# Kernel optimization log

Measured on AMD Instinct MI355X. Metric: run time of the kernel, lower is better.

The kernel has to match this reference:

```python
import jax, jax.numpy as jnp
import numpy as np

B, T, P, J, DIN, H, DOUT = 8, 64, 8, 32, 6, 256, 9
N = P * J


def _glorot(key, shape):
    fan_in, fan_out = shape[0], shape[1]
    s = jnp.sqrt(2.0 / (fan_in + fan_out)).astype(jnp.float32)
    return jax.random.normal(key, shape, jnp.float32) * s


def setup_inputs() -> dict:
    key = jax.random.key(0)
    ks = jax.random.split(key, 12)
    x2d = jax.random.normal(ks[0], (B, T, P, J, DIN), jnp.float32)
    mask = jnp.ones((B, T, P, J, 1), jnp.float32)
    # sparse-ish symmetric spatial adjacency with self loops, row-normalized
    a = (jax.random.uniform(ks[1], (N, N)) < 0.05).astype(jnp.float32)
    a = jnp.maximum(a, a.T) + jnp.eye(N, dtype=jnp.float32)
    s_adj = a / jnp.sum(a, axis=1, keepdims=True)
    return {
        "x2d": x2d,
        "mask": mask,
        "s_adj": s_adj,
        # layer 0: dim_in -> H, gates packed [z | r | c]
        "Wx0": _glorot(ks[2], (DIN, 3 * H)),
        "Wh0": _glorot(ks[3], (H, 3 * H)),
        "b0": jnp.zeros((3 * H,), jnp.float32),
        # layer 1: H -> H
        "Wx1": _glorot(ks[4], (H, 3 * H)),
        "Wh1": _glorot(ks[5], (H, 3 * H)),
        "b1": jnp.zeros((3 * H,), jnp.float32),
        # output head
        "Wout": _glorot(ks[6], (H, DOUT)),
        "bout": jnp.zeros((DOUT,), jnp.float32),
    }


def _gcgru_layer(xs, s_adj, Wx, Wh, b):
    """xs: [B, T, N, D] -> hidden sequence [B, T, N, H]."""
    h_dim = Wh.shape[0]

    def step(h, x_t):
        # graph conv of input and hidden state: A @ (.)
        Ax = jnp.einsum('nm,bmd->bnd', s_adj, x_t)          # [B,N,D]
        Ah = jnp.einsum('nm,bmh->bnh', s_adj, h)            # [B,N,H]
        gx = Ax @ Wx + b                                    # [B,N,3H]
        gzr = gx[..., : 2 * h_dim] + Ah @ Wh[:, : 2 * h_dim]
        z = jax.nn.sigmoid(gzr[..., :h_dim])                # update gate
        r = jax.nn.sigmoid(gzr[..., h_dim:])                # reset gate
        Arh = jnp.einsum('nm,bmh->bnh', s_adj, r * h)       # conv of reset hidden
        c = jnp.tanh(gx[..., 2 * h_dim:] + Arh @ Wh[:, 2 * h_dim:])
        h_new = z * h + (1.0 - z) * c
        return h_new, h_new

    h0 = jnp.zeros((xs.shape[0], xs.shape[2], h_dim), xs.dtype)
    _, hs = jax.lax.scan(step, h0, jnp.moveaxis(xs, 1, 0))  # hs: [T,B,N,H]
    return jnp.moveaxis(hs, 0, 1)


def reference(x2d, mask, s_adj, Wx0, Wh0, b0, Wx1, Wh1, b1, Wout, bout):
    bsz, seq_len, num_p, num_j, din = x2d.shape
    xs = (x2d * mask).reshape(bsz, seq_len, num_p * num_j, din)
    xs = _gcgru_layer(xs, s_adj, Wx0, Wh0, b0)
    xs = _gcgru_layer(xs, s_adj, Wx1, Wh1, b1)
    ys = xs @ Wout + bout                                   # [B,T,N,DOUT]
    return ys.reshape(bsz, seq_len, num_p, num_j, -1)
```

## Files before the change

### kernel.cpp

```cpp
#include <hip/hip_runtime.h>
#include <math.h>


#define BB 8
#define TT 64
#define NN 256
#define HH 256
#define BN 2048
#define LSTR 72

typedef float f32x4 __attribute__((ext_vector_type(4)));
typedef short s16x8 __attribute__((ext_vector_type(8)));

#define MFMA(a, b, c) __builtin_amdgcn_mfma_f32_16x16x32_bf16(a, b, c, 0, 0, 0)

__device__ __forceinline__ ushort rne_bf16(float x) {
    unsigned u = __builtin_bit_cast(unsigned, x);
    unsigned r = u + 0x7FFFu + ((u >> 16) & 1u);
    return (ushort)(r >> 16);
}
__device__ __forceinline__ float bf16_f32(ushort h) {
    unsigned u = ((unsigned)h) << 16;
    return __builtin_bit_cast(float, u);
}
__device__ __forceinline__ void split2(float x, ushort& hi, ushort& lo) {
    ushort h = rne_bf16(x);
    hi = h;
    lo = rne_bf16(x - bf16_f32(h));
}

__global__ __launch_bounds__(256) void prep_kernel(const float* __restrict__ A,
    const float* __restrict__ Wh0, const float* __restrict__ Wx1,
    const float* __restrict__ Wh1,
    ushort* Abf, ushort* WzrT0, ushort* WcT0, ushort* WxzrT1,
    ushort* WhzrT1, ushort* WxcT1, ushort* WhcT1)
{
    int idx = blockIdx.x * 256 + threadIdx.x;
    if (idx < 65536) { Abf[idx] = rne_bf16(A[idx]); return; }
    int e = idx - 65536;
    ushort* dst; const float* src; int colOff;
    if      (e < 131072) { dst = WzrT0;  src = Wh0; colOff = 0;   }
    else if (e < 196608) { dst = WcT0;   src = Wh0; colOff = 512; e -= 131072; }
    else if (e < 327680) { dst = WxzrT1; src = Wx1; colOff = 0;   e -= 196608; }
    else if (e < 458752) { dst = WhzrT1; src = Wh1; colOff = 0;   e -= 327680; }
    else if (e < 524288) { dst = WxcT1;  src = Wx1; colOff = 512; e -= 458752; }
    else if (e < 589824) { dst = WhcT1;  src = Wh1; colOff = 512; e -= 524288; }
    else return;
    int c = e >> 8, k = e & 255;
    dst[e] = rne_bf16(src[k * 768 + colOff + c]);
}

__device__ void x_job(int lb, int tid, float* xs, float* red, const float* Af,
                      const float* x2d, const float* mask, float* Ax0, int t) {
    int b = lb >> 2, rt = lb & 3;
    const float* xbase = x2d + ((size_t)(b * TT + t) * NN) * 6;
    const float* mbase = mask + (size_t)(b * TT + t) * NN;
    {
        int m = tid;
        float mk = mbase[m];
        #pragma unroll
        for (int d = 0; d < 6; ++d) xs[m * 8 + d] = xbase[m * 6 + d] * mk;
    }
    __syncthreads();
    int i = tid & 63, q = tid >> 6;
    const float* arow = Af + (size_t)(rt * 64 + i) * 256 + q * 64;
    float a6[6] = {0.f, 0.f, 0.f, 0.f, 0.f, 0.f};
    for (int m = 0; m < 64; ++m) {
        float a = arow[m];
        const float* xv = &xs[(q * 64 + m) * 8];
        #pragma unroll
        for (int d = 0; d < 6; ++d) a6[d] = fmaf(a, xv[d], a6[d]);
    }
    #pragma unroll
    for (int d = 0; d < 6; ++d) red[(i * 4 + q) * 8 + d] = a6[d];
    __syncthreads();
    for (int idx2 = tid; idx2 < 64 * 6; idx2 += 256) {
        int ii = idx2 / 6, d = idx2 - ii * 6;
        float s = red[(ii * 4 + 0) * 8 + d] + red[(ii * 4 + 1) * 8 + d]
                + red[(ii * 4 + 2) * 8 + d] + red[(ii * 4 + 3) * 8 + d];
        Ax0[(size_t)(b * 256 + rt * 64 + ii) * 8 + d] = s;
    }
}

__device__ void head_job(int lb, int tid, const float* h1, const float* Wout,
                         const float* bout, float* out, int tprev) {
    int g = lb * 256 + tid;
    int row = g / 9, o = g - row * 9;
    if (row >= BN) return;
    const float* hr = h1 + (size_t)row * 256;
    float s = bout[o];
    for (int k = 0; k < 256; k += 4) {
        float4 hv = *(const float4*)(hr + k);
        s = fmaf(hv.x, Wout[(k + 0) * 9 + o], s);
        s = fmaf(hv.y, Wout[(k + 1) * 9 + o], s);
        s = fmaf(hv.z, Wout[(k + 2) * 9 + o], s);
        s = fmaf(hv.w, Wout[(k + 3) * 9 + o], s);
    }
    int b = row >> 8, n = row & 255;
    out[((size_t)(b * TT + tprev) * NN + n) * 9 + o] = s;
}

__global__ __launch_bounds__(256) void head_kernel(const float* __restrict__ h1,
    const float* __restrict__ Wout, const float* __restrict__ bout,
    float* __restrict__ out, int tprev)
{
    head_job(blockIdx.x, threadIdx.x, h1, Wout, bout, out, tprev);
}

struct G2P {
    const ushort* Abf;
    const ushort* XThi0; const ushort* XTlo0; ushort* Yhi0; ushort* Ylo0;
    const ushort* XThi1; const ushort* XTlo1; ushort* Yhi1; ushort* Ylo1;
    int nJobs;
    int doX;
    int headT;
    int t;
    const float* Af; const float* x2d; const float* mask; float* Ax0;
    const float* h1; const float* Wout; const float* bout; float* out;
};

__global__ __launch_bounds__(256) void g2_kernel(G2P p) {
    __shared__ ushort lds[3 * 64 * LSTR];
    ushort* As   = lds;
    ushort* Bshi = lds + 64 * LSTR;
    ushort* Bslo = lds + 2 * 64 * LSTR;
    const int tid = threadIdx.x;
    const int bid = blockIdx.x;
    const int mainB = p.nJobs * 128;

    if (bid < mainB) {
        const int job = bid >> 7, lb = bid & 127;
        const ushort* XThi = job ? p.XThi1 : p.XThi0;
        const ushort* XTlo = job ? p.XTlo1 : p.XTlo0;
        ushort* Yhi = job ? p.Yhi1 : p.Yhi0;
        ushort* Ylo = job ? p.Ylo1 : p.Ylo0;
        const int b = lb >> 4, rt = (lb >> 2) & 3, ct = lb & 3;

        const int lane = tid & 63, wave = tid >> 6;
        const int wr = wave >> 1, wc = wave & 1;
        const int l15 = lane & 15, q8 = (lane >> 4) << 3;

        f32x4 acc[2][2];
        acc[0][0] = 0.f; acc[0][1] = 0.f; acc[1][0] = 0.f; acc[1][1] = 0.f;

        const int rr = tid >> 2, ko = (tid & 3) << 4;
        const ushort* Asrc = p.Abf + (size_t)(rt * 64 + rr) * 256 + ko;
        const ushort* Bh   = XThi + (size_t)(b * 256 + ct * 64 + rr) * 256 + ko;
        const ushort* Bl   = XTlo + (size_t)(b * 256 + ct * 64 + rr) * 256 + ko;
        ushort* wA = &As[rr * LSTR + ko];
        ushort* wH = &Bshi[rr * LSTR + ko];
        ushort* wL = &Bslo[rr * LSTR + ko];

        uint4 rA0 = *(const uint4*)(Asrc);
        uint4 rA1 = *(const uint4*)(Asrc + 8);
        uint4 rH0 = *(const uint4*)(Bh);
        uint4 rH1 = *(const uint4*)(Bh + 8);
        uint4 rL0 = *(const uint4*)(Bl);
        uint4 rL1 = *(const uint4*)(Bl + 8);

        for (int k0 = 0; k0 < 256; k0 += 64) {
            __syncthreads();
            *(uint4*)(wA)     = rA0;
            *(uint4*)(wA + 8) = rA1;
            *(uint4*)(wH)     = rH0;
            *(uint4*)(wH + 8) = rH1;
            *(uint4*)(wL)     = rL0;
            *(uint4*)(wL + 8) = rL1;
            __syncthreads();
            if (k0 < 192) {
                rA0 = *(const uint4*)(Asrc + k0 + 64);
                rA1 = *(const uint4*)(Asrc + k0 + 72);
                rH0 = *(const uint4*)(Bh + k0 + 64);
                rH1 = *(const uint4*)(Bh + k0 + 72);
                rL0 = *(const uint4*)(Bl + k0 + 64);
                rL1 = *(const uint4*)(Bl + k0 + 72);
            }
            #pragma unroll
            for (int sub = 0; sub < 2; ++sub) {
                const int kb = sub * 32 + q8;
                s16x8 a0  = *(const s16x8*)&As[(wr * 32 + l15) * LSTR + kb];
                s16x8 a1  = *(const s16x8*)&As[(wr * 32 + 16 + l15) * LSTR + kb];
                s16x8 bh0 = *(const s16x8*)&Bshi[(wc * 32 + l15) * LSTR + kb];
                s16x8 bh1 = *(const s16x8*)&Bshi[(wc * 32 + 16 + l15) * LSTR + kb];
                s16x8 bl0 = *(const s16x8*)&Bslo[(wc * 32 + l15) * LSTR + kb];
                s16x8 bl1 = *(const s16x8*)&Bslo[(wc * 32 + 16 + l15) * LSTR + kb];
                acc[0][0] = MFMA(a0, bh0, acc[0][0]);
                acc[0][0] = MFMA(a0, bl0, acc[0][0]);
                acc[0][1] = MFMA(a0, bh1, acc[0][1]);
                acc[0][1] = MFMA(a0, bl1, acc[0][1]);
                acc[1][0] = MFMA(a1, bh0, acc[1][0]);
                acc[1][0] = MFMA(a1, bl0, acc[1][0]);
                acc[1][1] = MFMA(a1, bh1, acc[1][1]);
                acc[1][1] = MFMA(a1, bl1, acc[1][1]);
            }
        }
        const int quad = lane >> 4;
        #pragma unroll
        for (int i = 0; i < 2; ++i) {
            #pragma unroll
            for (int j = 0; j < 2; ++j) {
                const int col = ct * 64 + wc * 32 + j * 16 + l15;
                const int m0  = rt * 64 + wr * 32 + i * 16 + quad * 4;
                const size_t base = (size_t)(b * 256 + m0) * 256 + col;
                #pragma unroll
                for (int r = 0; r < 4; ++r) {
                    ushort hi, lo;
                    split2(acc[i][j][r], hi, lo);
                    Yhi[base + (size_t)r * 256] = hi;
                    Ylo[base + (size_t)r * 256] = lo;
                }
            }
        }
    } else if (bid < mainB + 32) {
        if (p.doX)
            x_job(bid - mainB, tid, (float*)lds, (float*)(lds + 64 * LSTR),
                  p.Af, p.x2d, p.mask, p.Ax0, p.t);
    } else {
        if (p.headT >= 0)
            head_job(bid - mainB - 32, tid, p.h1, p.Wout, p.bout, p.out, p.headT);
    }
}

struct WSub {
    const ushort* Lhi0; const ushort* Llo0; const ushort* RT0;
    const ushort* Lhi1; const ushort* Llo1; const ushort* RT1;
    int ngemm;
    const float* bias;
    int useK6; int wxColOff;
    const float* h;
    float* z;
    float* hOut;
    ushort* Thi; ushort* Tlo;
};

struct WAP2 {
    WSub u0, u1;
    int nBlk0;
    int mode;
    const float* Ax0; const float* Wx0;
};

__global__ __launch_bounds__(256) void wact_kernel(WAP2 p) {
    __shared__ ushort lds[3 * 64 * LSTR];
    ushort* Ashi = lds;
    ushort* Aslo = lds + 64 * LSTR;
    ushort* Bs   = lds + 2 * 64 * LSTR;
    const int tid = threadIdx.x;
    const int bid = blockIdx.x;
    const int isU1 = (bid >= p.nBlk0);
    const WSub u = isU1 ? p.u1 : p.u0;
    const int lb = isU1 ? bid - p.nBlk0 : bid;
    int b, rt, ct;
    if (p.mode == 0) { b = lb >> 5; rt = (lb >> 3) & 3; ct = lb & 7; }
    else             { b = lb >> 4; rt = (lb >> 2) & 3; ct = lb & 3; }

    const int lane = tid & 63, wave = tid >> 6;
    const int wr = wave >> 1, wc = wave & 1;
    const int l15 = lane & 15, q8 = (lane >> 4) << 3;

    f32x4 acc[2][2];
    acc[0][0] = 0.f; acc[0][1] = 0.f; acc[1][0] = 0.f; acc[1][1] = 0.f;

    const int rr = tid >> 2, ko = (tid & 3) << 4;
    for (int g = 0; g < u.ngemm; ++g) {
        const ushort* Lh = (g ? u.Lhi1 : u.Lhi0) + (size_t)(b * 256 + rt * 64 + rr) * 256 + ko;
        const ushort* Ll = (g ? u.Llo1 : u.Llo0) + (size_t)(b * 256 + rt * 64 + rr) * 256 + ko;
        const ushort* Rt = (g ? u.RT1  : u.RT0 ) + (size_t)(ct * 64 + rr) * 256 + ko;
        ushort* wA = &Ashi[rr * LSTR + ko];
        ushort* wL = &Aslo[rr * LSTR + ko];
        ushort* wB = &Bs[rr * LSTR + ko];

        uint4 rA0 = *(const uint4*)(Lh);
        uint4 rA1 = *(const uint4*)(Lh + 8);
        uint4 rL0 = *(const uint4*)(Ll);
        uint4 rL1 = *(const uint4*)(Ll + 8);
        uint4 rB0 = *(const uint4*)(Rt);
        uint4 rB1 = *(const uint4*)(Rt + 8);

        for (int k0 = 0; k0 < 256; k0 += 64) {
            __syncthreads();
            *(uint4*)(wA)     = rA0;
            *(uint4*)(wA + 8) = rA1;
            *(uint4*)(wL)     = rL0;
            *(uint4*)(wL + 8) = rL1;
            *(uint4*)(wB)     = rB0;
            *(uint4*)(wB + 8) = rB1;
            __syncthreads();
            if (k0 < 192) {
                rA0 = *(const uint4*)(Lh + k0 + 64);
                rA1 = *(const uint4*)(Lh + k0 + 72);
                rL0 = *(const uint4*)(Ll + k0 + 64);
                rL1 = *(const uint4*)(Ll + k0 + 72);
                rB0 = *(const uint4*)(Rt + k0 + 64);
                rB1 = *(const uint4*)(Rt + k0 + 72);
            }
            #pragma unroll
            for (int sub = 0; sub < 2; ++sub) {
                const int kb = sub * 32 + q8;
                s16x8 ah0 = *(const s16x8*)&Ashi[(wr * 32 + l15) * LSTR + kb];
                s16x8 ah1 = *(const s16x8*)&Ashi[(wr * 32 + 16 + l15) * LSTR + kb];
                s16x8 al0 = *(const s16x8*)&Aslo[(wr * 32 + l15) * LSTR + kb];
                s16x8 al1 = *(const s16x8*)&Aslo[(wr * 32 + 16 + l15) * LSTR + kb];
                s16x8 b0  = *(const s16x8*)&Bs[(wc * 32 + l15) * LSTR + kb];
                s16x8 b1  = *(const s16x8*)&Bs[(wc * 32 + 16 + l15) * LSTR + kb];
                acc[0][0] = MFMA(ah0, b0, acc[0][0]);
                acc[0][0] = MFMA(al0, b0, acc[0][0]);
                acc[0][1] = MFMA(ah0, b1, acc[0][1]);
                acc[0][1] = MFMA(al0, b1, acc[0][1]);
                acc[1][0] = MFMA(ah1, b0, acc[1][0]);
                acc[1][0] = MFMA(al1, b0, acc[1][0]);
                acc[1][1] = MFMA(ah1, b1, acc[1][1]);
                acc[1][1] = MFMA(al1, b1, acc[1][1]);
            }
        }
    }

    const int quad = lane >> 4;
    const int m0base = rt * 64 + wr * 32;
    int colg[2];
    #pragma unroll
    for (int j = 0; j < 2; ++j) colg[j] = ct * 64 + wc * 32 + j * 16 + l15;
    float bv[2] = { u.bias[colg[0]], u.bias[colg[1]] };
    float v[2][2][4];
    #pragma unroll
    for (int i = 0; i < 2; ++i)
        #pragma unroll
        for (int j = 0; j < 2; ++j)
            #pragma unroll
            for (int r = 0; r < 4; ++r)
                v[i][j][r] = acc[i][j][r] + bv[j];

    if (u.useK6) {
        float w6[2][6];
        #pragma unroll
        for (int j = 0; j < 2; ++j)
            #pragma unroll
            for (int d = 0; d < 6; ++d)
                w6[j][d] = p.Wx0[d * 768 + u.wxColOff + colg[j]];
        #pragma unroll
        for (int i = 0; i < 2; ++i) {
            #pragma unroll
            for (int r = 0; r < 4; ++r) {
                int row = b * 256 + m0base + i * 16 + quad * 4 + r;
                const float* ax = p.Ax0 + (size_t)row * 8;
                float a0 = ax[0], a1 = ax[1], a2 = ax[2], a3 = ax[3], a4 = ax[4], a5 = ax[5];
                #pragma unroll
                for (int j = 0; j < 2; ++j)
                    v[i][j][r] += a0 * w6[j][0] + a1 * w6[j][1] + a2 * w6[j][2]
                                + a3 * w6[j][3] + a4 * w6[j][4] + a5 * w6[j][5];
            }
        }
    }

    if (p.mode == 0) {
        if (ct < 4) {
            #pragma unroll
            for (int i = 0; i < 2; ++i)
                #pragma unroll
                for (int r = 0; r < 4; ++r) {
                    int row = b * 256 + m0base + i * 16 + quad * 4 + r;
                    #pragma unroll
                    for (int j = 0; j < 2; ++j)
                        u.z[(size_t)row * 256 + colg[j]] = 1.f / (1.f + __expf(-v[i][j][r]));
                }
        } else {
            #pragma unroll
            for (int i = 0; i < 2; ++i) {
                int m0 = m0base + i * 16 + quad * 4;
                #pragma unroll
                for (int j = 0; j < 2; ++j) {
                    int colp = colg[j] - 256;
                    ushort hi4[4], lo4[4];
                    #pragma unroll
                    for (int r = 0; r < 4; ++r) {
                        int row = b * 256 + m0 + r;
                        float s = 1.f / (1.f + __expf(-v[i][j][r]));
                        float rh = s * u.h[(size_t)row * 256 + colp];
                        split2(rh, hi4[r], lo4[r]);
                    }
                    size_t off = (size_t)b * 65536 + (size_t)colp * 256 + m0;
                    *(ushort4*)&u.Thi[off] = make_ushort4(hi4[0], hi4[1], hi4[2], hi4[3]);
                    *(ushort4*)&u.Tlo[off] = make_ushort4(lo4[0], lo4[1], lo4[2], lo4[3]);
                }
            }
        }
    } else {
        #pragma unroll
        for (int i = 0; i < 2; ++i) {
            int m0 = m0base + i * 16 + quad * 4;
            #pragma unroll
            for (int j = 0; j < 2; ++j) {
                ushort hi4[4], lo4[4];
                #pragma unroll
                for (int r = 0; r < 4; ++r) {
                    int row = b * 256 + m0 + r;
                    size_t gi = (size_t)row * 256 + colg[j];
                    float c = tanhf(v[i][j][r]);
                    float zz = u.z[gi];
                    float hh = u.h[gi];
                    float hn = zz * hh + (1.f - zz) * c;
                    u.hOut[gi] = hn;
                    split2(hn, hi4[r], lo4[r]);
                }
                size_t off = (size_t)b * 65536 + (size_t)colg[j] * 256 + m0;
                *(ushort4*)&u.Thi[off] = make_ushort4(hi4[0], hi4[1], hi4[2], hi4[3]);
                *(ushort4*)&u.Tlo[off] = make_ushort4(lo4[0], lo4[1], lo4[2], lo4[3]);
            }
        }
    }
}

extern "C" void kernel_launch(void* const* d_in, const int* in_sizes, int n_in,
                              void* d_out, int out_size, void* d_ws, size_t ws_size,
                              hipStream_t stream) {
    const float* x2d  = (const float*)d_in[0];
    const float* mask = (const float*)d_in[1];
    const float* A    = (const float*)d_in[2];
    const float* Wx0  = (const float*)d_in[3];
    const float* Wh0  = (const float*)d_in[4];
    const float* b0   = (const float*)d_in[5];
    const float* Wx1  = (const float*)d_in[6];
    const float* Wh1  = (const float*)d_in[7];
    const float* b1   = (const float*)d_in[8];
    const float* Wout = (const float*)d_in[9];
    const float* bout = (const float*)d_in[10];
    float* out = (float*)d_out;

    const size_t SZ = (size_t)BN * HH;
    float* ws = (float*)d_ws;
    float*  h0    = ws;
    float*  h1    = h0 + SZ;
    ushort* h0Thi = (ushort*)(h1 + SZ);
    ushort* h0Tlo = h0Thi + SZ;
    ushort* h1Thi = h0Tlo + SZ;
    ushort* h1Tlo = h1Thi + SZ;
    float*  z0    = (float*)(h1Tlo + SZ);
    float*  z1    = z0 + SZ;
    float*  Ax0   = z1 + SZ;
    ushort* AH0hi = (ushort*)(Ax0 + 16384);
    ushort* AH0lo = AH0hi + SZ;
    ushort* AH1hi = AH0lo + SZ;
    ushort* AH1lo = AH1hi + SZ;
    ushort* ARH1hi= AH1lo + SZ;
    ushort* ARH1lo= ARH1hi + SZ;
    ushort* RH0Thi= ARH1lo + SZ;
    ushort* RH0Tlo= RH0Thi + SZ;
    ushort* RH1Thi= RH0Tlo + SZ;
    ushort* RH1Tlo= RH1Thi + SZ;
    ushort* Abf   = RH1Tlo + SZ;
    ushort* WzrT0 = Abf + 65536;
    ushort* WcT0  = WzrT0 + 131072;
    ushort* WxzrT1= WcT0 + 65536;
    ushort* WhzrT1= WxzrT1 + 131072;
    ushort* WxcT1 = WhzrT1 + 131072;
    ushort* WhcT1 = WxcT1 + 65536;
    ushort* ARH0hi = AH1hi;
    ushort* ARH0lo = AH1lo;

    hipMemsetAsync(h0, 0, (2 * SZ) * sizeof(float) + 4 * SZ * sizeof(ushort), stream);

    prep_kernel<<<dim3(2560), dim3(256), 0, stream>>>(A, Wh0, Wx1, Wh1,
        Abf, WzrT0, WcT0, WxzrT1, WhzrT1, WxcT1, WhcT1);

    for (int s = 0; s <= TT; ++s) {
        const int L0 = (s < TT);
        const int L1 = (s >= 1);

        { G2P p{Abf, h0Thi, h0Tlo, AH0hi, AH0lo, h1Thi, h1Tlo, AH1hi, AH1lo,
                2, L0, (s >= 2 ? s - 2 : -1), s,
                A, x2d, mask, Ax0, h1, Wout, bout, out};
          g2_kernel<<<dim3(360), dim3(256), 0, stream>>>(p); }

        { WAP2 p;
          p.u0 = WSub{AH0hi, AH0lo, WzrT0, nullptr, nullptr, nullptr, 1,
                      b0, 1, 0, h0, z0, nullptr, RH0Thi, RH0Tlo};
          p.u1 = WSub{AH0hi, AH0lo, WxzrT1, AH1hi, AH1lo, WhzrT1, 2,
                      b1, 0, 0, h1, z1, nullptr, RH1Thi, RH1Tlo};
          p.mode = 0; p.Ax0 = Ax0; p.Wx0 = Wx0;
          int g;
          if (L0 && L1) { p.nBlk0 = 256; g = 512; }
          else if (L0)  { p.nBlk0 = 256; g = 256; }
          else          { p.nBlk0 = 0;   g = 256; }
          wact_kernel<<<dim3(g), dim3(256), 0, stream>>>(p); }

        { G2P p{Abf,
                L0 ? RH0Thi : RH1Thi, L0 ? RH0Tlo : RH1Tlo,
                L0 ? ARH0hi : ARH1hi, L0 ? ARH0lo : ARH1lo,
                RH1Thi, RH1Tlo, ARH1hi, ARH1lo,
                (L0 && L1) ? 2 : 1, 0, -1, s,
                A, x2d, mask, Ax0, h1, Wout, bout, out};
          g2_kernel<<<dim3(((L0 && L1) ? 2 : 1) * 128), dim3(256), 0, stream>>>(p); }

        { WAP2 p;
          p.u0 = WSub{ARH0hi, ARH0lo, WcT0, nullptr, nullptr, nullptr, 1,
                      b0 + 512, 1, 512, h0, z0, h0, h0Thi, h0Tlo};
          p.u1 = WSub{ARH1hi, ARH1lo, WhcT1, AH0hi, AH0lo, WxcT1, 2,
                      b1 + 512, 0, 0, h1, z1, h1, h1Thi, h1Tlo};
          p.mode = 1; p.Ax0 = Ax0; p.Wx0 = Wx0;
          int g;
          if (L0 && L1) { p.nBlk0 = 128; g = 256; }
          else if (L0)  { p.nBlk0 = 128; g = 128; }
          else          { p.nBlk0 = 0;   g = 128; }
          wact_kernel<<<dim3(g), dim3(256), 0, stream>>>(p); }
    }

    head_kernel<<<dim3(72), dim3(256), 0, stream>>>(h1, Wout, bout, out, TT - 1);
}
```

Before: 3.301 ms.

## Fuse reset-gate compute with A·(r*h) graph conv in one kernel

Replaces the separate z/r gate kernel and the following graph-conv kernel for r*h with a single launch. Some blocks compute only the z gate, while new blocks recompute the r-gate columns for a 32-feature slice over all nodes, form r*h in LDS and multiply by the adjacency directly. This removes one launch per step and the global round trip for the transposed r*h buffers. In exchange the r-gate GEMM is recomputed per feature slice, and the parallelism of the conv stage changes to 64 blocks per layer.

```diff
diff --git a/kernel.cpp b/kernel.cpp
--- a/kernel.cpp
+++ b/kernel.cpp
@@ -233,26 +233,12 @@
     ushort* Thi; ushort* Tlo;
 };
 
-struct WAP2 {
-    WSub u0, u1;
-    int nBlk0;
-    int mode;
-    const float* Ax0; const float* Wx0;
-};
-
-__global__ __launch_bounds__(256) void wact_kernel(WAP2 p) {
-    __shared__ ushort lds[3 * 64 * LSTR];
+__device__ void wact_body(int b, int rt, int ct, int tid, ushort* lds,
+                          const WSub& u, int mode, const float* Ax0,
+                          const float* Wx0) {
     ushort* Ashi = lds;
     ushort* Aslo = lds + 64 * LSTR;
     ushort* Bs   = lds + 2 * 64 * LSTR;
-    const int tid = threadIdx.x;
-    const int bid = blockIdx.x;
-    const int isU1 = (bid >= p.nBlk0);
-    const WSub u = isU1 ? p.u1 : p.u0;
-    const int lb = isU1 ? bid - p.nBlk0 : bid;
-    int b, rt, ct;
-    if (p.mode == 0) { b = lb >> 5; rt = (lb >> 3) & 3; ct = lb & 7; }
-    else             { b = lb >> 4; rt = (lb >> 2) & 3; ct = lb & 3; }
 
     const int lane = tid & 63, wave = tid >> 6;
     const int wr = wave >> 1, wc = wave & 1;
@@ -336,13 +322,13 @@
         for (int j = 0; j < 2; ++j)
             #pragma unroll
             for (int d = 0; d < 6; ++d)
-                w6[j][d] = p.Wx0[d * 768 + u.wxColOff + colg[j]];
+                w6[j][d] = Wx0[d * 768 + u.wxColOff + colg[j]];
         #pragma unroll
         for (int i = 0; i < 2; ++i) {
             #pragma unroll
             for (int r = 0; r < 4; ++r) {
                 int row = b * 256 + m0base + i * 16 + quad * 4 + r;
-                const float* ax = p.Ax0 + (size_t)row * 8;
+                const float* ax = Ax0 + (size_t)row * 8;
                 float a0 = ax[0], a1 = ax[1], a2 = ax[2], a3 = ax[3], a4 = ax[4], a5 = ax[5];
                 #pragma unroll
                 for (int j = 0; j < 2; ++j)
@@ -352,38 +338,16 @@
         }
     }
 
-    if (p.mode == 0) {
-        if (ct < 4) {
-            #pragma unroll
-            for (int i = 0; i < 2; ++i)
+    if (mode == 0) {
+        #pragma unroll
+        for (int i = 0; i < 2; ++i)
+            #pragma unroll
+            for (int r = 0; r < 4; ++r) {
+                int row = b * 256 + m0base + i * 16 + quad * 4 + r;
                 #pragma unroll
-                for (int r = 0; r < 4; ++r) {
-                    int row = b * 256 + m0base + i * 16 + quad * 4 + r;
-                    #pragma unroll
-                    for (int j = 0; j < 2; ++j)
-                        u.z[(size_t)row * 256 + colg[j]] = 1.f / (1.f + __expf(-v[i][j][r]));
-                }
-        } else {
-            #pragma unroll
-            for (int i = 0; i < 2; ++i) {
-                int m0 = m0base + i * 16 + quad * 4;
-                #pragma unroll
-                for (int j = 0; j < 2; ++j) {
-                    int colp = colg[j] - 256;
-                    ushort hi4[4], lo4[4];
-                    #pragma unroll
-                    for (int r = 0; r < 4; ++r) {
-                        int row = b * 256 + m0 + r;
-                        float s = 1.f / (1.f + __expf(-v[i][j][r]));
-                        float rh = s * u.h[(size_t)row * 256 + colp];
-                        split2(rh, hi4[r], lo4[r]);
-                    }
-                    size_t off = (size_t)b * 65536 + (size_t)colp * 256 + m0;
-                    *(ushort4*)&u.Thi[off] = make_ushort4(hi4[0], hi4[1], hi4[2], hi4[3]);
-                    *(ushort4*)&u.Tlo[off] = make_ushort4(lo4[0], lo4[1], lo4[2], lo4[3]);
-                }
-            }
-        }
+                for (int j = 0; j < 2; ++j)
+                    u.z[(size_t)row * 256 + colg[j]] = 1.f / (1.f + __expf(-v[i][j][r]));
+            }
     } else {
         #pragma unroll
         for (int i = 0; i < 2; ++i) {
@@ -407,6 +371,231 @@
                 *(ushort4*)&u.Tlo[off] = make_ushort4(lo4[0], lo4[1], lo4[2], lo4[3]);
             }
         }
+    }
+}
+
+struct WAP2 {
+    WSub u0, u1;
+    int nBlk0;
+    int mode;
+    const float* Ax0; const float* Wx0;
+};
+
+__global__ __launch_bounds__(256) void wact_kernel(WAP2 p) {
+    __shared__ ushort lds[3 * 64 * LSTR];
+    const int tid = threadIdx.x;
+    const int bid = blockIdx.x;
+    const int isU1 = (bid >= p.nBlk0);
+    const WSub u = isU1 ? p.u1 : p.u0;
+    const int lb = isU1 ? bid - p.nBlk0 : bid;
+    int b, rt, ct;
+    if (p.mode == 0) { b = lb >> 5; rt = (lb >> 3) & 3; ct = lb & 7; }
+    else             { b = lb >> 4; rt = (lb >> 2) & 3; ct = lb & 3; }
+    wact_body(b, rt, ct, tid, lds, u, p.mode, p.Ax0, p.Wx0);
+}
+
+struct KP2 {
+    const ushort* Abf;
+    const ushort* AH0hi; const ushort* AH0lo;
+    const ushort* AH1hi; const ushort* AH1lo;
+    const ushort* WzrT0; const ushort* WxzrT1; const ushort* WhzrT1;
+    const float* b0; const float* b1;
+    const float* Ax0; const float* Wx0;
+    const ushort* h0Thi; const ushort* h0Tlo;
+    const ushort* h1Thi; const ushort* h1Tlo;
+    float* z0; float* z1;
+    ushort* ARH0hi; ushort* ARH0lo;
+    ushort* ARH1hi; ushort* ARH1lo;
+    int L0; int L1;
+};
+
+#define CS 72
+#define RS 264
+
+__device__ void rh_job(int ell, int b, int fp, int tid, ushort* lds, const KP2& q) {
+    ushort* WTa  = lds;
+    ushort* WTb  = lds + 32 * CS;
+    ushort* rhHi = lds + 2 * 32 * CS;
+    ushort* rhLo = rhHi + 32 * RS;
+
+    const int F0 = fp * 32;
+    const ushort* WT0 = ell ? q.WxzrT1 : q.WzrT0;
+    const ushort* WT1 = q.WhzrT1;
+    const ushort* B0h = q.AH0hi; const ushort* B0l = q.AH0lo;
+    const ushort* B1h = q.AH1hi; const ushort* B1l = q.AH1lo;
+    const float*  bias = ell ? q.b1 : q.b0;
+    const ushort* hThi = ell ? q.h1Thi : q.h0Thi;
+    const ushort* hTlo = ell ? q.h1Tlo : q.h0Tlo;
+    ushort* Yhi = ell ? q.ARH1hi : q.ARH0hi;
+    ushort* Ylo = ell ? q.ARH1lo : q.ARH0lo;
+
+    const int lane = tid & 63, wave = tid >> 6;
+    const int l15 = lane & 15, q8 = (lane >> 4) << 3, quad = lane >> 4;
+
+    f32x4 acc[2][2][2];
+    #pragma unroll
+    for (int a = 0; a < 2; ++a)
+        #pragma unroll
+        for (int i = 0; i < 2; ++i)
+            #pragma unroll
+            for (int j = 0; j < 2; ++j) acc[a][i][j] = 0.f;
+
+    const int srow = tid >> 3, skoff = (tid & 7) << 3;
+    for (int k0 = 0; k0 < 256; k0 += 64) {
+        __syncthreads();
+        *(uint4*)&WTa[srow * CS + skoff] =
+            *(const uint4*)&WT0[(size_t)(256 + F0 + srow) * 256 + k0 + skoff];
+        if (ell)
+            *(uint4*)&WTb[srow * CS + skoff] =
+                *(const uint4*)&WT1[(size_t)(256 + F0 + srow) * 256 + k0 + skoff];
+        __syncthreads();
+        #pragma unroll
+        for (int msub = 0; msub < 2; ++msub) {
+            const int m0 = wave * 64 + msub * 32;
+            const size_t gb0 = (size_t)(b * 256 + m0 + l15) * 256 + k0;
+            const size_t gb1 = (size_t)(b * 256 + m0 + 16 + l15) * 256 + k0;
+            #pragma unroll
+            for (int sub = 0; sub < 2; ++sub) {
+                const int kb = sub * 32 + q8;
+                s16x8 a0 = *(const s16x8*)&WTa[l15 * CS + kb];
+                s16x8 a1 = *(const s16x8*)&WTa[(16 + l15) * CS + kb];
+                s16x8 bh0 = *(const s16x8*)&B0h[gb0 + kb];
+                s16x8 bh1 = *(const s16x8*)&B0h[gb1 + kb];
+                s16x8 bl0 = *(const s16x8*)&B0l[gb0 + kb];
+                s16x8 bl1 = *(const s16x8*)&B0l[gb1 + kb];
+                acc[msub][0][0] = MFMA(a0, bh0, acc[msub][0][0]);
+                acc[msub][0][0] = MFMA(a0, bl0, acc[msub][0][0]);
+                acc[msub][0][1] = MFMA(a0, bh1, acc[msub][0][1]);
+                acc[msub][0][1] = MFMA(a0, bl1, acc[msub][0][1]);
+                acc[msub][1][0] = MFMA(a1, bh0, acc[msub][1][0]);
+                acc[msub][1][0] = MFMA(a1, bl0, acc[msub][1][0]);
+                acc[msub][1][1] = MFMA(a1, bh1, acc[msub][1][1]);
+                acc[msub][1][1] = MFMA(a1, bl1, acc[msub][1][1]);
+                if (ell) {
+                    s16x8 c0 = *(const s16x8*)&WTb[l15 * CS + kb];
+                    s16x8 c1 = *(const s16x8*)&WTb[(16 + l15) * CS + kb];
+                    s16x8 dh0 = *(const s16x8*)&B1h[gb0 + kb];
+                    s16x8 dh1 = *(const s16x8*)&B1h[gb1 + kb];
+                    s16x8 dl0 = *(const s16x8*)&B1l[gb0 + kb];
+                    s16x8 dl1 = *(const s16x8*)&B1l[gb1 + kb];
+                    acc[msub][0][0] = MFMA(c0, dh0, acc[msub][0][0]);
+                    acc[msub][0][0] = MFMA(c0, dl0, acc[msub][0][0]);
+                    acc[msub][0][1] = MFMA(c0, dh1, acc[msub][0][1]);
+                    acc[msub][0][1] = MFMA(c0, dl1, acc[msub][0][1]);
+                    acc[msub][1][0] = MFMA(c1, dh0, acc[msub][1][0]);
+                    acc[msub][1][0] = MFMA(c1, dl0, acc[msub][1][0]);
+                    acc[msub][1][1] = MFMA(c1, dh1, acc[msub][1][1]);
+                    acc[msub][1][1] = MFMA(c1, dl1, acc[msub][1][1]);
+                }
+            }
+        }
+    }
+
+    float w6[2][4][6];
+    if (!ell) {
+        #pragma unroll
+        for (int i = 0; i < 2; ++i)
+            #pragma unroll
+            for (int r = 0; r < 4; ++r) {
+                const int f = i * 16 + quad * 4 + r;
+                #pragma unroll
+                for (int d = 0; d < 6; ++d)
+                    w6[i][r][d] = q.Wx0[d * 768 + 256 + F0 + f];
+            }
+    }
+    #pragma unroll
+    for (int msub = 0; msub < 2; ++msub) {
+        #pragma unroll
+        for (int j = 0; j < 2; ++j) {
+            const int m = wave * 64 + msub * 32 + j * 16 + l15;
+            float ax[6];
+            if (!ell) {
+                const float* axp = q.Ax0 + (size_t)(b * 256 + m) * 8;
+                #pragma unroll
+                for (int d = 0; d < 6; ++d) ax[d] = axp[d];
+            }
+            #pragma unroll
+            for (int i = 0; i < 2; ++i)
+                #pragma unroll
+                for (int r = 0; r < 4; ++r) {
+                    const int f = i * 16 + quad * 4 + r;
+                    float v = acc[msub][i][j][r] + bias[256 + F0 + f];
+                    if (!ell)
+                        v += ax[0] * w6[i][r][0] + ax[1] * w6[i][r][1]
+                           + ax[2] * w6[i][r][2] + ax[3] * w6[i][r][3]
+                           + ax[4] * w6[i][r][4] + ax[5] * w6[i][r][5];
+                    float rr = 1.f / (1.f + __expf(-v));
+                    const size_t hoff = (size_t)b * 65536 + (size_t)(F0 + f) * 256 + m;
+                    float hv = bf16_f32(hThi[hoff]) + bf16_f32(hTlo[hoff]);
+                    ushort hi, lo;
+                    split2(rr * hv, hi, lo);
+                    rhHi[f * RS + m] = hi;
+                    rhLo[f * RS + m] = lo;
+                }
+        }
+    }
+    __syncthreads();
+
+    f32x4 acc2[4][2];
+    #pragma unroll
+    for (int i = 0; i < 4; ++i) { acc2[i][0] = 0.f; acc2[i][1] = 0.f; }
+    const int n0 = wave * 64;
+    for (int mc = 0; mc < 256; mc += 32) {
+        const int kb = mc + q8;
+        s16x8 a0 = *(const s16x8*)&q.Abf[(size_t)(n0 +      l15) * 256 + kb];
+        s16x8 a1 = *(const s16x8*)&q.Abf[(size_t)(n0 + 16 + l15) * 256 + kb];
+        s16x8 a2 = *(const s16x8*)&q.Abf[(size_t)(n0 + 32 + l15) * 256 + kb];
+        s16x8 a3 = *(const s16x8*)&q.Abf[(size_t)(n0 + 48 + l15) * 256 + kb];
+        s16x8 bh0 = *(const s16x8*)&rhHi[l15 * RS + kb];
+        s16x8 bh1 = *(const s16x8*)&rhHi[(16 + l15) * RS + kb];
+        s16x8 bl0 = *(const s16x8*)&rhLo[l15 * RS + kb];
+        s16x8 bl1 = *(const s16x8*)&rhLo[(16 + l15) * RS + kb];
+        acc2[0][0] = MFMA(a0, bh0, acc2[0][0]); acc2[0][0] = MFMA(a0, bl0, acc2[0][0]);
+        acc2[0][1] = MFMA(a0, bh1, acc2[0][1]); acc2[0][1] = MFMA(a0, bl1, acc2[0][1]);
+        acc2[1][0] = MFMA(a1, bh0, acc2[1][0]); acc2[1][0] = MFMA(a1, bl0, acc2[1][0]);
+        acc2[1][1] = MFMA(a1, bh1, acc2[1][1]); acc2[1][1] = MFMA(a1, bl1, acc2[1][1]);
+        acc2[2][0] = MFMA(a2, bh0, acc2[2][0]); acc2[2][0] = MFMA(a2, bl0, acc2[2][0]);
+        acc2[2][1] = MFMA(a2, bh1, acc2[2][1]); acc2[2][1] = MFMA(a2, bl1, acc2[2][1]);
+        acc2[3][0] = MFMA(a3, bh0, acc2[3][0]); acc2[3][0] = MFMA(a3, bl0, acc2[3][0]);
+        acc2[3][1] = MFMA(a3, bh1, acc2[3][1]); acc2[3][1] = MFMA(a3, bl1, acc2[3][1]);
+    }
+    #pragma unroll
+    for (int i = 0; i < 4; ++i) {
+        #pragma unroll
+        for (int j = 0; j < 2; ++j) {
+            const int n = n0 + i * 16 + quad * 4;
+            const int col = F0 + j * 16 + l15;
+            const size_t base = (size_t)(b * 256 + n) * 256 + col;
+            #pragma unroll
+            for (int r = 0; r < 4; ++r) {
+                ushort hi, lo;
+                split2(acc2[i][j][r], hi, lo);
+                Yhi[base + (size_t)r * 256] = hi;
+                Ylo[base + (size_t)r * 256] = lo;
+            }
+        }
+    }
+}
+
+__global__ __launch_bounds__(256) void karb_kernel(KP2 q) {
+    __shared__ ushort lds[2 * 32 * CS + 2 * 32 * RS];
+    const int bid = blockIdx.x, tid = threadIdx.x;
+    if (bid < 256) {
+        const int ell = bid >> 7, lb = bid & 127;
+        if (ell ? !q.L1 : !q.L0) return;
+        const int b = lb >> 4, rt = (lb >> 2) & 3, ct = lb & 3;
+        WSub u;
+        if (ell) u = WSub{q.AH0hi, q.AH0lo, q.WxzrT1, q.AH1hi, q.AH1lo, q.WhzrT1,
+                          2, q.b1, 0, 0, nullptr, q.z1, nullptr, nullptr, nullptr};
+        else     u = WSub{q.AH0hi, q.AH0lo, q.WzrT0, nullptr, nullptr, nullptr,
+                          1, q.b0, 1, 0, nullptr, q.z0, nullptr, nullptr, nullptr};
+        wact_body(b, rt, ct, tid, lds, u, 0, q.Ax0, q.Wx0);
+    } else {
+        const int idx = bid - 256;
+        const int ell = idx >> 6;
+        if (ell ? !q.L1 : !q.L0) return;
+        const int b = (idx >> 3) & 7, fp = idx & 7;
+        rh_job(ell, b, fp, tid, lds, q);
     }
 }
 
@@ -443,19 +632,17 @@
     ushort* AH1lo = AH1hi + SZ;
     ushort* ARH1hi= AH1lo + SZ;
     ushort* ARH1lo= ARH1hi + SZ;
-    ushort* RH0Thi= ARH1lo + SZ;
-    ushort* RH0Tlo= RH0Thi + SZ;
-    ushort* RH1Thi= RH0Tlo + SZ;
-    ushort* RH1Tlo= RH1Thi + SZ;
-    ushort* Abf   = RH1Tlo + SZ;
+    ushort* ARH0hi= ARH1lo + SZ;
+    ushort* ARH0lo= ARH0hi + SZ;
+    ushort* unus1 = ARH0lo + SZ;
+    ushort* unus2 = unus1 + SZ;
+    ushort* Abf   = unus2 + SZ;
     ushort* WzrT0 = Abf + 65536;
     ushort* WcT0  = WzrT0 + 131072;
     ushort* WxzrT1= WcT0 + 65536;
     ushort* WhzrT1= WxzrT1 + 131072;
     ushort* WxcT1 = WhzrT1 + 131072;
     ushort* WhcT1 = WxcT1 + 65536;
-    ushort* ARH0hi = AH1hi;
-    ushort* ARH0lo = AH1lo;
 
     hipMemsetAsync(h0, 0, (2 * SZ) * sizeof(float) + 4 * SZ * sizeof(ushort), stream);
 
@@ -471,25 +658,17 @@
                 A, x2d, mask, Ax0, h1, Wout, bout, out};
           g2_kernel<<<dim3(360), dim3(256), 0, stream>>>(p); }
 
-        { WAP2 p;
-          p.u0 = WSub{AH0hi, AH0lo, WzrT0, nullptr, nullptr, nullptr, 1,
-                      b0, 1, 0, h0, z0, nullptr, RH0Thi, RH0Tlo};
-          p.u1 = WSub{AH0hi, AH0lo, WxzrT1, AH1hi, AH1lo, WhzrT1, 2,
-                      b1, 0, 0, h1, z1, nullptr, RH1Thi, RH1Tlo};
-          p.mode = 0; p.Ax0 = Ax0; p.Wx0 = Wx0;
-          int g;
-          if (L0 && L1) { p.nBlk0 = 256; g = 512; }
-          else if (L0)  { p.nBlk0 = 256; g = 256; }
-          else          { p.nBlk0 = 0;   g = 256; }
-          wact_kernel<<<dim3(g), dim3(256), 0, stream>>>(p); }
-
-        { G2P p{Abf,
-                L0 ? RH0Thi : RH1Thi, L0 ? RH0Tlo : RH1Tlo,
-                L0 ? ARH0hi : ARH1hi, L0 ? ARH0lo : ARH1lo,
-                RH1Thi, RH1Tlo, ARH1hi, ARH1lo,
-                (L0 && L1) ? 2 : 1, 0, -1, s,
-                A, x2d, mask, Ax0, h1, Wout, bout, out};
-          g2_kernel<<<dim3(((L0 && L1) ? 2 : 1) * 128), dim3(256), 0, stream>>>(p); }
+        { KP2 q;
+          q.Abf = Abf;
+          q.AH0hi = AH0hi; q.AH0lo = AH0lo; q.AH1hi = AH1hi; q.AH1lo = AH1lo;
+          q.WzrT0 = WzrT0; q.WxzrT1 = WxzrT1; q.WhzrT1 = WhzrT1;
+          q.b0 = b0; q.b1 = b1; q.Ax0 = Ax0; q.Wx0 = Wx0;
+          q.h0Thi = h0Thi; q.h0Tlo = h0Tlo; q.h1Thi = h1Thi; q.h1Tlo = h1Tlo;
+          q.z0 = z0; q.z1 = z1;
+          q.ARH0hi = ARH0hi; q.ARH0lo = ARH0lo;
+          q.ARH1hi = ARH1hi; q.ARH1lo = ARH1lo;
+          q.L0 = L0; q.L1 = L1;
+          karb_kernel<<<dim3(384), dim3(256), 0, stream>>>(q); }
 
         { WAP2 p;
           p.u0 = WSub{ARH0hi, ARH0lo, WcT0, nullptr, nullptr, nullptr, 1,
```

Result: slower. 3.969 ms (+20.3%).
